# Optimization experiments

Hardware: AMD Instinct MI355X
Metric: run time of the kernel (lower is better)

Reference implementation:

```python
import jax, jax.numpy as jnp
import numpy as np

N_NODES = 30000
N_EDGES = 480000
IN_FEATS = 256
H_FEATS = 128
HEADS = 4
OUT_DIM = 128
NEG_SLOPE = 0.2  # PyG GATConv default leaky_relu slope


def gat_conv(x, src, dst, W, att_src, att_dst, bias, concat):
    """PyG-style GATConv (eval mode, self-loops already in src/dst).
    x: [N, Fin]; W: [Fin, H*C]; att_src/att_dst: [H, C]; bias: [H*C] or [C].
    """
    N = x.shape[0]
    H, C = att_src.shape
    h = (x @ W).reshape(N, H, C)                       # [N, H, C]
    a_src = jnp.einsum('nhc,hc->nh', h, att_src)       # [N, H]
    a_dst = jnp.einsum('nhc,hc->nh', h, att_dst)
    e = jax.nn.leaky_relu(a_src[src] + a_dst[dst], NEG_SLOPE)  # [E, H]
    # segment softmax over incoming edges of each dst node
    m = jax.ops.segment_max(e, dst, num_segments=N)    # [N, H]
    m = jnp.where(jnp.isfinite(m), m, 0.0)
    ex = jnp.exp(e - m[dst])
    denom = jax.ops.segment_sum(ex, dst, num_segments=N)
    alpha = ex / denom[dst]                            # [E, H]
    msg = alpha[:, :, None] * h[src]                   # [E, H, C]
    out = jax.ops.segment_sum(msg, dst, num_segments=N)  # [N, H, C]
    if concat:
        out = out.reshape(N, H * C)
    else:
        out = out.mean(axis=1)
    return out + bias


def setup_inputs() -> dict:
    key = jax.random.key(0)
    ks = jax.random.split(key, 12)
    s = 0.05
    x = jax.random.normal(ks[0], (N_NODES, IN_FEATS), dtype=jnp.float32)
    edge_index = jax.random.randint(ks[1], (2, N_EDGES), 0, N_NODES, dtype=jnp.int64)
    W1 = jax.random.normal(ks[2], (IN_FEATS, HEADS * H_FEATS), dtype=jnp.float32) * s
    att_src1 = jax.random.normal(ks[3], (HEADS, H_FEATS), dtype=jnp.float32) * s
    att_dst1 = jax.random.normal(ks[4], (HEADS, H_FEATS), dtype=jnp.float32) * s
    b1 = jnp.zeros((HEADS * H_FEATS,), dtype=jnp.float32)
    W2 = jax.random.normal(ks[5], (HEADS * H_FEATS, HEADS * H_FEATS), dtype=jnp.float32) * s
    att_src2 = jax.random.normal(ks[6], (HEADS, H_FEATS), dtype=jnp.float32) * s
    att_dst2 = jax.random.normal(ks[7], (HEADS, H_FEATS), dtype=jnp.float32) * s
    b2 = jnp.zeros((HEADS * H_FEATS,), dtype=jnp.float32)
    W3 = jax.random.normal(ks[8], (HEADS * H_FEATS, OUT_DIM), dtype=jnp.float32) * s
    att_src3 = jax.random.normal(ks[9], (1, OUT_DIM), dtype=jnp.float32) * s
    att_dst3 = jax.random.normal(ks[10], (1, OUT_DIM), dtype=jnp.float32) * s
    b3 = jnp.zeros((OUT_DIM,), dtype=jnp.float32)
    return {"x": x, "edge_index": edge_index,
            "W1": W1, "att_src1": att_src1, "att_dst1": att_dst1, "b1": b1,
            "W2": W2, "att_src2": att_src2, "att_dst2": att_dst2, "b2": b2,
            "W3": W3, "att_src3": att_src3, "att_dst3": att_dst3, "b3": b3}


def reference(x, edge_index, W1, att_src1, att_dst1, b1,
              W2, att_src2, att_dst2, b2, W3, att_src3, att_dst3, b3):
    # PyG GATConv adds self-loops by default
    loops = jnp.arange(N_NODES, dtype=edge_index.dtype)
    src = jnp.concatenate([edge_index[0], loops])
    dst = jnp.concatenate([edge_index[1], loops])
    h = gat_conv(x, src, dst, W1, att_src1, att_dst1, b1, concat=True)
    h = jax.nn.relu(h)  # dropout inactive in eval mode
    h = gat_conv(h, src, dst, W2, att_src2, att_dst2, b2, concat=True)
    h = jax.nn.relu(h)
    out = gat_conv(h, src, dst, W3, att_src3, att_dst3, b3, concat=False)
    return out
```

## Files before the change

### kernel.cpp

```cpp
#include <hip/hip_runtime.h>


#define NEG_SLOPE 0.2f

typedef __attribute__((ext_vector_type(8))) short short8;
typedef __attribute__((ext_vector_type(4))) float floatx4;

static __device__ __forceinline__ unsigned short f2bf(float f) {
    unsigned u = __float_as_uint(f);
    u = u + 0x7FFFu + ((u >> 16) & 1u);
    return (unsigned short)(u >> 16);
}
static __device__ __forceinline__ float bf2f_lo(unsigned u) {
    return __uint_as_float(u << 16);
}
static __device__ __forceinline__ float bf2f_hi(unsigned u) {
    return __uint_as_float(u & 0xFFFF0000u);
}

static __device__ __forceinline__ void async_copy16(const void* g, void* l) {
    __builtin_amdgcn_global_load_lds(
        (const __attribute__((address_space(1))) unsigned int*)g,
        (__attribute__((address_space(3))) unsigned int*)l, 16, 0, 0);
}


__global__ __launch_bounds__(256)
void cast_bf16_kernel(const float* __restrict__ in, unsigned short* __restrict__ out, int n4) {
    int i = blockIdx.x * 256 + threadIdx.x;
    if (i < n4) {
        float4 v = ((const float4*)in)[i];
        ushort4 o;
        o.x = f2bf(v.x); o.y = f2bf(v.y); o.z = f2bf(v.z); o.w = f2bf(v.w);
        ((ushort4*)out)[i] = o;
    }
}

__global__ __launch_bounds__(256)
void wt_kernel(const float* __restrict__ W, unsigned short* __restrict__ WT, int K, int N) {
    int idx = blockIdx.x * 256 + threadIdx.x;
    if (idx < K * N) {
        int k = idx / N, n = idx - k * N;
        WT[(size_t)n * K + k] = f2bf(W[idx]);
    }
}


__global__ __launch_bounds__(256)
void init_counts_kernel(int* cursor, int N) {
    int i = blockIdx.x * 256 + threadIdx.x;
    if (i < N) cursor[i] = 1;
}

__global__ __launch_bounds__(256)
void hist_kernel(const int* __restrict__ ei, int* cursor, int E) {
    int e = blockIdx.x * 256 + threadIdx.x;
    if (e < E) atomicAdd(&cursor[ei[E + e]], 1);
}

__global__ __launch_bounds__(1024)
void scan_kernel(int* __restrict__ cursor, int* __restrict__ row_ptr, int N) {
    __shared__ int wsum[16];
    __shared__ int carry_sh;
    int tid = threadIdx.x, lane = tid & 63, w = tid >> 6;
    if (tid == 0) carry_sh = 0;
    __syncthreads();
    for (int base = 0; base < N; base += 1024) {
        int i = base + tid;
        int v = (i < N) ? cursor[i] : 0;
        int x = v;
        #pragma unroll
        for (int off = 1; off < 64; off <<= 1) {
            int t = __shfl_up(x, off, 64);
            if (lane >= off) x += t;
        }
        if (lane == 63) wsum[w] = x;
        __syncthreads();
        if (w == 0 && lane < 16) {
            int y = wsum[lane];
            #pragma unroll
            for (int off = 1; off < 16; off <<= 1) {
                int t = __shfl_up(y, off, 64);
                if (lane >= off) y += t;
            }
            wsum[lane] = y;
        }
        __syncthreads();
        int woff = (w == 0) ? 0 : wsum[w - 1];
        int carry = carry_sh;
        int incl = x + woff;
        if (i < N) { int ex = carry + incl - v; row_ptr[i] = ex; cursor[i] = ex; }
        __syncthreads();
        if (tid == 1023) carry_sh = carry + incl;
        __syncthreads();
    }
    if (tid == 0) row_ptr[N] = carry_sh;
}

__global__ __launch_bounds__(256)
void scatter_kernel(const int* __restrict__ ei, int* cursor,
                    int* __restrict__ csr_src, int E, int N) {
    int i = blockIdx.x * 256 + threadIdx.x;
    if (i < E) {
        int s = ei[i], d = ei[E + i];
        int pos = atomicAdd(&cursor[d], 1);
        csr_src[pos] = s;
    } else if (i < E + N) {
        int n = i - E;
        int pos = atomicAdd(&cursor[n], 1);
        csr_src[pos] = n;
    }
}


template<bool BF16OUT>
__global__ __launch_bounds__(256)
void mfma_gemm_kernel(const unsigned short* __restrict__ A,
                      const unsigned short* __restrict__ BT,
                      void* __restrict__ C_v, int M, int Nn, int K) {
    __shared__ unsigned short As[128 * 32];
    __shared__ unsigned short Bs[128 * 32];
    const int tid = threadIdx.x;
    const int m0 = blockIdx.y * 128;
    const int n0 = blockIdx.x * 128;
    const int lane = tid & 63, wave = tid >> 6;
    const int wm = (wave & 1) * 64, wn = (wave >> 1) * 64;
    const int quad = lane >> 4, rr = lane & 15;

    const int r16 = lane >> 2;
    const int phys = lane & 3;
    const int rowL0 = wave * 32 + r16;
    const int rowL1 = wave * 32 + 16 + r16;
    const int seg0 = phys ^ ((rowL0 >> 1) & 3);
    const int seg1 = phys ^ ((rowL1 >> 1) & 3);
    const int gmA0 = min(m0 + rowL0, M - 1);
    const int gmA1 = min(m0 + rowL1, M - 1);
    const int gnB0 = n0 + rowL0;
    const int gnB1 = n0 + rowL1;
    unsigned short* ldsA0 = As + (wave * 32) * 32;
    unsigned short* ldsA1 = As + (wave * 32 + 16) * 32;
    unsigned short* ldsB0 = Bs + (wave * 32) * 32;
    unsigned short* ldsB1 = Bs + (wave * 32 + 16) * 32;

    const int swz = quad ^ ((rr >> 1) & 3);

    floatx4 acc[4][4] = {};

    for (int k0 = 0; k0 < K; k0 += 32) {
        async_copy16(A  + (size_t)gmA0 * K + k0 + seg0 * 8, ldsA0);
        async_copy16(A  + (size_t)gmA1 * K + k0 + seg1 * 8, ldsA1);
        async_copy16(BT + (size_t)gnB0 * K + k0 + seg0 * 8, ldsB0);
        async_copy16(BT + (size_t)gnB1 * K + k0 + seg1 * 8, ldsB1);
        __syncthreads();

        short8 af[4], bf[4];
        #pragma unroll
        for (int mi = 0; mi < 4; ++mi)
            af[mi] = *(const short8*)(As + (wm + mi * 16 + rr) * 32 + swz * 8);
        #pragma unroll
        for (int ni = 0; ni < 4; ++ni)
            bf[ni] = *(const short8*)(Bs + (wn + ni * 16 + rr) * 32 + swz * 8);
        #pragma unroll
        for (int mi = 0; mi < 4; ++mi)
            #pragma unroll
            for (int ni = 0; ni < 4; ++ni)
                acc[mi][ni] = __builtin_amdgcn_mfma_f32_16x16x32_bf16(
                    af[mi], bf[ni], acc[mi][ni], 0, 0, 0);
        __syncthreads();
    }

    #pragma unroll
    for (int mi = 0; mi < 4; ++mi) {
        #pragma unroll
        for (int ni = 0; ni < 4; ++ni) {
            int col = n0 + wn + ni * 16 + rr;
            #pragma unroll
            for (int r = 0; r < 4; ++r) {
                int row = m0 + wm + mi * 16 + quad * 4 + r;
                if (row < M) {
                    if (BF16OUT)
                        ((unsigned short*)C_v)[(size_t)row * Nn + col] = f2bf(acc[mi][ni][r]);
                    else
                        ((float*)C_v)[(size_t)row * Nn + col] = acc[mi][ni][r];
                }
            }
        }
    }
}


template<int H>
__global__ __launch_bounds__(256)
void attdot_kernel(const unsigned* __restrict__ hfeat, const float* __restrict__ att_src,
                   const float* __restrict__ att_dst, float* __restrict__ a_src,
                   float* __restrict__ a_dst, int N) {
    constexpr int C = 128;
    constexpr int F = H * C;
    constexpr int UPL = F / 128;
    constexpr int G = C / (2 * UPL);
    int wave = threadIdx.x >> 6, lane = threadIdx.x & 63;
    int n = blockIdx.x * 4 + wave;
    if (n >= N) return;
    const int myh = (2 * UPL * lane) / C;
    const int cbase = (2 * UPL * lane) & (C - 1);

    unsigned u[UPL];
    if (UPL == 4) {
        uint4 t = ((const uint4*)(hfeat + (size_t)n * (F / 2)))[lane];
        u[0] = t.x; u[1] = t.y; u[2] = t.z; u[3] = t.w;
    } else {
        u[0] = hfeat[(size_t)n * (F / 2) + lane];
    }
    float s = 0.f, d = 0.f;
    #pragma unroll
    for (int q = 0; q < UPL; ++q) {
        float v0 = bf2f_lo(u[q]), v1 = bf2f_hi(u[q]);
        int c = cbase + 2 * q;
        s += v0 * att_src[myh * C + c] + v1 * att_src[myh * C + c + 1];
        d += v0 * att_dst[myh * C + c] + v1 * att_dst[myh * C + c + 1];
    }
    #pragma unroll
    for (int off = G / 2; off; off >>= 1) {
        s += __shfl_xor(s, off, 64);
        d += __shfl_xor(d, off, 64);
    }
    if ((lane & (G - 1)) == 0) {
        a_src[n * H + myh] = s;
        a_dst[n * H + myh] = d;
    }
}


template<int F, int H, bool RELU, bool BF16OUT>
__global__ __launch_bounds__(256)
void agg_kernel(const unsigned* __restrict__ hfeat, const float* __restrict__ a_src,
                const float* __restrict__ a_dst, const int* __restrict__ row_ptr,
                const int* __restrict__ csr_src, const float* __restrict__ bias,
                void* __restrict__ out_v, int N) {
    constexpr int C = 128;
    constexpr int UPL = F / 128;
    constexpr int RU = F / 2;
    const int wave = threadIdx.x >> 6, lane = threadIdx.x & 63;
    const int n = blockIdx.x * 4 + wave;
    if (n >= N) return;
    const int begin = row_ptr[n];
    const int deg = row_ptr[n + 1] - begin;
    const int myh = (2 * UPL * lane) / C;
    const float adst = a_dst[n * H + myh];

    float acc[2 * UPL];
    #pragma unroll
    for (int j = 0; j < 2 * UPL; ++j) acc[j] = 0.f;
    float dacc = 0.f;

    unsigned uA[UPL], uB[UPL];
    float avA = 0.f, avB = 0.f;

#define LOADSLOT(idx, U, AV)                                              \
    {                                                                     \
        int s_ = csr_src[begin + (idx)];                                  \
        if (UPL == 4) {                                                   \
            uint4 t_ = ((const uint4*)(hfeat + (size_t)s_ * RU))[lane];   \
            U[0] = t_.x; U[1] = t_.y; U[2] = t_.z; U[3] = t_.w;           \
        } else {                                                          \
            U[0] = hfeat[(size_t)s_ * RU + lane];                         \
        }                                                                 \
        AV = a_src[s_ * H + myh];                                         \
    }

#define CONSUME(U, AV)                                                    \
    {                                                                     \
        float e_ = AV + adst;                                             \
        e_ = e_ > 0.f ? e_ : NEG_SLOPE * e_;                              \
        float ex_ = __expf(e_);                                           \
        dacc += ex_;                                                      \
        _Pragma("unroll")                                                 \
        for (int q_ = 0; q_ < UPL; ++q_) {                                \
            acc[2 * q_]     += ex_ * bf2f_lo(U[q_]);                      \
            acc[2 * q_ + 1] += ex_ * bf2f_hi(U[q_]);                      \
        }                                                                 \
    }

    LOADSLOT(0, uA, avA);
    if (deg > 1) LOADSLOT(1, uB, avB);
    int i = 0;
    for (; i + 4 <= deg; i += 2) {
        CONSUME(uA, avA);
        LOADSLOT(i + 2, uA, avA);
        CONSUME(uB, avB);
        LOADSLOT(i + 3, uB, avB);
    }
    int rem = deg - i;
    CONSUME(uA, avA);
    if (rem == 3) {
        LOADSLOT(i + 2, uA, avA);
        CONSUME(uB, avB);
        CONSUME(uA, avA);
    } else if (rem == 2) {
        CONSUME(uB, avB);
    }
#undef LOADSLOT
#undef CONSUME

    float inv = 1.f / dacc;
    const int cb = 2 * UPL * lane;
    if (BF16OUT) {
        unsigned pk[UPL];
        #pragma unroll
        for (int q = 0; q < UPL; ++q) {
            float v0 = acc[2 * q] * inv + bias[cb + 2 * q];
            float v1 = acc[2 * q + 1] * inv + bias[cb + 2 * q + 1];
            if (RELU) { v0 = fmaxf(v0, 0.f); v1 = fmaxf(v1, 0.f); }
            pk[q] = (unsigned)f2bf(v0) | ((unsigned)f2bf(v1) << 16);
        }
        if (UPL == 4) {
            uint4 t; t.x = pk[0]; t.y = pk[1]; t.z = pk[2]; t.w = pk[3];
            ((uint4*)((unsigned*)out_v + (size_t)n * RU))[lane] = t;
        } else {
            ((unsigned*)out_v)[(size_t)n * RU + lane] = pk[0];
        }
    } else {
        #pragma unroll
        for (int q = 0; q < UPL; ++q) {
            float v0 = acc[2 * q] * inv + bias[cb + 2 * q];
            float v1 = acc[2 * q + 1] * inv + bias[cb + 2 * q + 1];
            if (RELU) { v0 = fmaxf(v0, 0.f); v1 = fmaxf(v1, 0.f); }
            float2 o; o.x = v0; o.y = v1;
            ((float2*)((float*)out_v + (size_t)n * F))[UPL * lane + q] = o;
        }
    }
}


extern "C" void kernel_launch(void* const* d_in, const int* in_sizes, int n_in,
                              void* d_out, int out_size, void* d_ws, size_t ws_size,
                              hipStream_t stream) {
    const float* x        = (const float*)d_in[0];
    const int*   ei       = (const int*)  d_in[1];
    const float* W1       = (const float*)d_in[2];
    const float* att_src1 = (const float*)d_in[3];
    const float* att_dst1 = (const float*)d_in[4];
    const float* b1       = (const float*)d_in[5];
    const float* W2       = (const float*)d_in[6];
    const float* att_src2 = (const float*)d_in[7];
    const float* att_dst2 = (const float*)d_in[8];
    const float* b2       = (const float*)d_in[9];
    const float* W3       = (const float*)d_in[10];
    const float* att_src3 = (const float*)d_in[11];
    const float* att_dst3 = (const float*)d_in[12];
    const float* b3       = (const float*)d_in[13];

    const int IN_FEATS = 256;
    const int N = in_sizes[0] / IN_FEATS;
    const int E = in_sizes[1] / 2;
    const int ET = E + N;

    char* p = (char*)d_ws;
    unsigned short* h_bf    = (unsigned short*)p; p += (size_t)N * 512 * sizeof(unsigned short);
    unsigned short* act_bf  = (unsigned short*)p; p += (size_t)N * 512 * sizeof(unsigned short);
    unsigned short* x_bf    = (unsigned short*)p; p += (size_t)N * 256 * sizeof(unsigned short);
    float*          a_src   = (float*)p;          p += (size_t)N * 4 * sizeof(float);
    float*          a_dst   = (float*)p;          p += (size_t)N * 4 * sizeof(float);
    unsigned short* W_T     = (unsigned short*)p; p += (size_t)512 * 512 * sizeof(unsigned short);
    int*            row_ptr = (int*)p;            p += ((size_t)N + 16) * sizeof(int);
    int*            cursor  = (int*)p;            p += ((size_t)N + 16) * sizeof(int);
    int*            csr_src = (int*)p;            p += (size_t)ET * sizeof(int);

    init_counts_kernel<<<(N + 255) / 256, 256, 0, stream>>>(cursor, N);
    hist_kernel<<<(E + 255) / 256, 256, 0, stream>>>(ei, cursor, E);
    scan_kernel<<<1, 1024, 0, stream>>>(cursor, row_ptr, N);
    scatter_kernel<<<(E + N + 255) / 256, 256, 0, stream>>>(ei, cursor, csr_src, E, N);

    {
        int n4 = N * 256 / 4;
        cast_bf16_kernel<<<(n4 + 255) / 256, 256, 0, stream>>>(x, x_bf, n4);
    }

    const int MB = (N + 127) / 128;
    const int NB4 = (N + 3) / 4;

    wt_kernel<<<(256 * 512 + 255) / 256, 256, 0, stream>>>(W1, W_T, 256, 512);
    mfma_gemm_kernel<true><<<dim3(4, MB), 256, 0, stream>>>(x_bf, W_T, h_bf, N, 512, 256);
    attdot_kernel<4><<<NB4, 256, 0, stream>>>((const unsigned*)h_bf, att_src1, att_dst1, a_src, a_dst, N);
    agg_kernel<512, 4, true, true><<<NB4, 256, 0, stream>>>((const unsigned*)h_bf, a_src, a_dst, row_ptr, csr_src, b1, act_bf, N);

    wt_kernel<<<(512 * 512 + 255) / 256, 256, 0, stream>>>(W2, W_T, 512, 512);
    mfma_gemm_kernel<true><<<dim3(4, MB), 256, 0, stream>>>(act_bf, W_T, h_bf, N, 512, 512);
    attdot_kernel<4><<<NB4, 256, 0, stream>>>((const unsigned*)h_bf, att_src2, att_dst2, a_src, a_dst, N);
    agg_kernel<512, 4, true, true><<<NB4, 256, 0, stream>>>((const unsigned*)h_bf, a_src, a_dst, row_ptr, csr_src, b2, act_bf, N);

    wt_kernel<<<(512 * 128 + 255) / 256, 256, 0, stream>>>(W3, W_T, 512, 128);
    mfma_gemm_kernel<true><<<dim3(1, MB), 256, 0, stream>>>(act_bf, W_T, h_bf, N, 128, 512);
    attdot_kernel<1><<<NB4, 256, 0, stream>>>((const unsigned*)h_bf, att_src3, att_dst3, a_src, a_dst, N);
    agg_kernel<128, 1, false, false><<<NB4, 256, 0, stream>>>((const unsigned*)h_bf, a_src, a_dst, row_ptr, csr_src, b3, d_out, N);
}
```

Measured before the change: 448.8 us.

## Parallelize CSR scan, fuse attention dots into GEMM, deepen aggregation prefetch

Replaces the single-block serial prefix scan with a three-kernel multi-block scan (block sums, block offsets, final scan). Fuses the attention-coefficient dot products into the GEMM epilogue using fp32 accumulators, which removes the attdot kernels and their re-read of h. In the aggregation kernel, neighbour prefetch grows from two slots to four, and scalar readfirstlane is applied to row pointers and source indices. The block-offset kernel assumes at most 64 scan blocks, and the fused epilogue adds shared memory and shuffle work to the GEMM.

```diff
diff --git a/kernel.cpp b/kernel.cpp
--- a/kernel.cpp
+++ b/kernel.cpp
@@ -59,42 +59,66 @@
 }
 
 __global__ __launch_bounds__(1024)
-void scan_kernel(int* __restrict__ cursor, int* __restrict__ row_ptr, int N) {
+void scan_bsum_kernel(const int* __restrict__ cursor, int* __restrict__ bsum, int N) {
     __shared__ int wsum[16];
-    __shared__ int carry_sh;
     int tid = threadIdx.x, lane = tid & 63, w = tid >> 6;
-    if (tid == 0) carry_sh = 0;
+    int i = blockIdx.x * 1024 + tid;
+    int v = (i < N) ? cursor[i] : 0;
+    #pragma unroll
+    for (int off = 32; off; off >>= 1) v += __shfl_xor(v, off, 64);
+    if (lane == 0) wsum[w] = v;
     __syncthreads();
-    for (int base = 0; base < N; base += 1024) {
-        int i = base + tid;
-        int v = (i < N) ? cursor[i] : 0;
-        int x = v;
-        #pragma unroll
-        for (int off = 1; off < 64; off <<= 1) {
-            int t = __shfl_up(x, off, 64);
-            if (lane >= off) x += t;
-        }
-        if (lane == 63) wsum[w] = x;
-        __syncthreads();
-        if (w == 0 && lane < 16) {
-            int y = wsum[lane];
-            #pragma unroll
-            for (int off = 1; off < 16; off <<= 1) {
-                int t = __shfl_up(y, off, 64);
-                if (lane >= off) y += t;
-            }
-            wsum[lane] = y;
-        }
-        __syncthreads();
-        int woff = (w == 0) ? 0 : wsum[w - 1];
-        int carry = carry_sh;
-        int incl = x + woff;
-        if (i < N) { int ex = carry + incl - v; row_ptr[i] = ex; cursor[i] = ex; }
-        __syncthreads();
-        if (tid == 1023) carry_sh = carry + incl;
-        __syncthreads();
-    }
-    if (tid == 0) row_ptr[N] = carry_sh;
+    if (tid == 0) {
+        int t = 0;
+        #pragma unroll
+        for (int k = 0; k < 16; ++k) t += wsum[k];
+        bsum[blockIdx.x] = t;
+    }
+}
+
+__global__ __launch_bounds__(64)
+void scan_boffs_kernel(const int* __restrict__ bsum, int* __restrict__ boffs,
+                       int NB, int* __restrict__ row_ptr, int N) {
+    int lane = threadIdx.x;
+    int v = (lane < NB) ? bsum[lane] : 0;
+    int x = v;
+    #pragma unroll
+    for (int off = 1; off < 64; off <<= 1) {
+        int t = __shfl_up(x, off, 64);
+        if (lane >= off) x += t;
+    }
+    if (lane < NB) boffs[lane] = x - v;
+    if (lane == 63) row_ptr[N] = x;
+}
+
+__global__ __launch_bounds__(1024)
+void scan_final_kernel(int* __restrict__ cursor, const int* __restrict__ boffs,
+                       int* __restrict__ row_ptr, int N) {
+    __shared__ int wsum[16];
+    int tid = threadIdx.x, lane = tid & 63, w = tid >> 6;
+    int i = blockIdx.x * 1024 + tid;
+    int v = (i < N) ? cursor[i] : 0;
+    int x = v;
+    #pragma unroll
+    for (int off = 1; off < 64; off <<= 1) {
+        int t = __shfl_up(x, off, 64);
+        if (lane >= off) x += t;
+    }
+    if (lane == 63) wsum[w] = x;
+    __syncthreads();
+    if (w == 0 && lane < 16) {
+        int y = wsum[lane];
+        #pragma unroll
+        for (int off = 1; off < 16; off <<= 1) {
+            int t = __shfl_up(y, off, 64);
+            if (lane >= off) y += t;
+        }
+        wsum[lane] = y;
+    }
+    __syncthreads();
+    int woff = (w == 0) ? 0 : wsum[w - 1];
+    int ex = boffs[blockIdx.x] + woff + x - v;
+    if (i < N) { row_ptr[i] = ex; cursor[i] = ex; }
 }
 
 __global__ __launch_bounds__(256)
@@ -113,16 +137,22 @@
 }
 
 
-template<bool BF16OUT>
 __global__ __launch_bounds__(256)
 void mfma_gemm_kernel(const unsigned short* __restrict__ A,
                       const unsigned short* __restrict__ BT,
-                      void* __restrict__ C_v, int M, int Nn, int K) {
+                      unsigned short* __restrict__ C,
+                      const float* __restrict__ att_src,
+                      const float* __restrict__ att_dst,
+                      float* __restrict__ a_srcO, float* __restrict__ a_dstO,
+                      int H, int M, int Nn, int K) {
     __shared__ unsigned short As[128 * 32];
     __shared__ unsigned short Bs[128 * 32];
+    __shared__ float psum[2][128];
+    __shared__ float pdsum[2][128];
     const int tid = threadIdx.x;
     const int m0 = blockIdx.y * 128;
     const int n0 = blockIdx.x * 128;
+    const int head = blockIdx.x;
     const int lane = tid & 63, wave = tid >> 6;
     const int wm = (wave & 1) * 64, wn = (wave >> 1) * 64;
     const int quad = lane >> 4, rr = lane & 15;
@@ -177,56 +207,48 @@
             #pragma unroll
             for (int r = 0; r < 4; ++r) {
                 int row = m0 + wm + mi * 16 + quad * 4 + r;
-                if (row < M) {
-                    if (BF16OUT)
-                        ((unsigned short*)C_v)[(size_t)row * Nn + col] = f2bf(acc[mi][ni][r]);
-                    else
-                        ((float*)C_v)[(size_t)row * Nn + col] = acc[mi][ni][r];
-                }
+                if (row < M) C[(size_t)row * Nn + col] = f2bf(acc[mi][ni][r]);
             }
         }
     }
-}
-
-
-template<int H>
-__global__ __launch_bounds__(256)
-void attdot_kernel(const unsigned* __restrict__ hfeat, const float* __restrict__ att_src,
-                   const float* __restrict__ att_dst, float* __restrict__ a_src,
-                   float* __restrict__ a_dst, int N) {
-    constexpr int C = 128;
-    constexpr int F = H * C;
-    constexpr int UPL = F / 128;
-    constexpr int G = C / (2 * UPL);
-    int wave = threadIdx.x >> 6, lane = threadIdx.x & 63;
-    int n = blockIdx.x * 4 + wave;
-    if (n >= N) return;
-    const int myh = (2 * UPL * lane) / C;
-    const int cbase = (2 * UPL * lane) & (C - 1);
-
-    unsigned u[UPL];
-    if (UPL == 4) {
-        uint4 t = ((const uint4*)(hfeat + (size_t)n * (F / 2)))[lane];
-        u[0] = t.x; u[1] = t.y; u[2] = t.z; u[3] = t.w;
-    } else {
-        u[0] = hfeat[(size_t)n * (F / 2) + lane];
-    }
-    float s = 0.f, d = 0.f;
-    #pragma unroll
-    for (int q = 0; q < UPL; ++q) {
-        float v0 = bf2f_lo(u[q]), v1 = bf2f_hi(u[q]);
-        int c = cbase + 2 * q;
-        s += v0 * att_src[myh * C + c] + v1 * att_src[myh * C + c + 1];
-        d += v0 * att_dst[myh * C + c] + v1 * att_dst[myh * C + c + 1];
-    }
-    #pragma unroll
-    for (int off = G / 2; off; off >>= 1) {
-        s += __shfl_xor(s, off, 64);
-        d += __shfl_xor(d, off, 64);
-    }
-    if ((lane & (G - 1)) == 0) {
-        a_src[n * H + myh] = s;
-        a_dst[n * H + myh] = d;
+
+    float ats[4], atd[4];
+    #pragma unroll
+    for (int ni = 0; ni < 4; ++ni) {
+        int c = wn + ni * 16 + rr;
+        ats[ni] = att_src[head * 128 + c];
+        atd[ni] = att_dst[head * 128 + c];
+    }
+    const int wnh = wn >> 6;
+    #pragma unroll
+    for (int mi = 0; mi < 4; ++mi) {
+        #pragma unroll
+        for (int r = 0; r < 4; ++r) {
+            float ps = 0.f, pd = 0.f;
+            #pragma unroll
+            for (int ni = 0; ni < 4; ++ni) {
+                ps += ats[ni] * acc[mi][ni][r];
+                pd += atd[ni] * acc[mi][ni][r];
+            }
+            #pragma unroll
+            for (int off = 1; off < 16; off <<= 1) {
+                ps += __shfl_xor(ps, off, 64);
+                pd += __shfl_xor(pd, off, 64);
+            }
+            if (rr == 0) {
+                int row = wm + mi * 16 + quad * 4 + r;
+                psum[wnh][row] = ps;
+                pdsum[wnh][row] = pd;
+            }
+        }
+    }
+    __syncthreads();
+    if (tid < 128) {
+        int gr = m0 + tid;
+        if (gr < M) {
+            a_srcO[(size_t)gr * H + head] = psum[0][tid] + psum[1][tid];
+            a_dstO[(size_t)gr * H + head] = pdsum[0][tid] + pdsum[1][tid];
+        }
     }
 }
 
@@ -243,8 +265,8 @@
     const int wave = threadIdx.x >> 6, lane = threadIdx.x & 63;
     const int n = blockIdx.x * 4 + wave;
     if (n >= N) return;
-    const int begin = row_ptr[n];
-    const int deg = row_ptr[n + 1] - begin;
+    const int begin = __builtin_amdgcn_readfirstlane(row_ptr[n]);
+    const int deg = __builtin_amdgcn_readfirstlane(row_ptr[n + 1]) - begin;
     const int myh = (2 * UPL * lane) / C;
     const float adst = a_dst[n * H + myh];
 
@@ -253,12 +275,12 @@
     for (int j = 0; j < 2 * UPL; ++j) acc[j] = 0.f;
     float dacc = 0.f;
 
-    unsigned uA[UPL], uB[UPL];
-    float avA = 0.f, avB = 0.f;
+    unsigned u0[UPL], u1[UPL], u2[UPL], u3[UPL];
+    float av0 = 0.f, av1 = 0.f, av2 = 0.f, av3 = 0.f;
 
 #define LOADSLOT(idx, U, AV)                                              \
     {                                                                     \
-        int s_ = csr_src[begin + (idx)];                                  \
+        int s_ = __builtin_amdgcn_readfirstlane(csr_src[begin + (idx)]);  \
         if (UPL == 4) {                                                   \
             uint4 t_ = ((const uint4*)(hfeat + (size_t)s_ * RU))[lane];   \
             U[0] = t_.x; U[1] = t_.y; U[2] = t_.z; U[3] = t_.w;           \
@@ -281,24 +303,25 @@
         }                                                                 \
     }
 
-    LOADSLOT(0, uA, avA);
-    if (deg > 1) LOADSLOT(1, uB, avB);
+    LOADSLOT(0, u0, av0);
+    if (deg > 1) LOADSLOT(1, u1, av1);
+    if (deg > 2) LOADSLOT(2, u2, av2);
+    if (deg > 3) LOADSLOT(3, u3, av3);
     int i = 0;
-    for (; i + 4 <= deg; i += 2) {
-        CONSUME(uA, avA);
-        LOADSLOT(i + 2, uA, avA);
-        CONSUME(uB, avB);
-        LOADSLOT(i + 3, uB, avB);
+    for (; i + 8 <= deg; i += 4) {
+        CONSUME(u0, av0); LOADSLOT(i + 4, u0, av0);
+        CONSUME(u1, av1); LOADSLOT(i + 5, u1, av1);
+        CONSUME(u2, av2); LOADSLOT(i + 6, u2, av2);
+        CONSUME(u3, av3); LOADSLOT(i + 7, u3, av3);
     }
     int rem = deg - i;
-    CONSUME(uA, avA);
-    if (rem == 3) {
-        LOADSLOT(i + 2, uA, avA);
-        CONSUME(uB, avB);
-        CONSUME(uA, avA);
-    } else if (rem == 2) {
-        CONSUME(uB, avB);
-    }
+    CONSUME(u0, av0); if (rem > 4) LOADSLOT(i + 4, u0, av0);
+    if (rem > 1) { CONSUME(u1, av1); if (rem > 5) LOADSLOT(i + 5, u1, av1); }
+    if (rem > 2) { CONSUME(u2, av2); if (rem > 6) LOADSLOT(i + 6, u2, av2); }
+    if (rem > 3) CONSUME(u3, av3);
+    if (rem > 4) CONSUME(u0, av0);
+    if (rem > 5) CONSUME(u1, av1);
+    if (rem > 6) CONSUME(u2, av2);
 #undef LOADSLOT
 #undef CONSUME
 
@@ -354,6 +377,7 @@
     const int N = in_sizes[0] / IN_FEATS;
     const int E = in_sizes[1] / 2;
     const int ET = E + N;
+    const int NB = (N + 1023) / 1024;
 
     char* p = (char*)d_ws;
     unsigned short* h_bf    = (unsigned short*)p; p += (size_t)N * 512 * sizeof(unsigned short);
@@ -364,11 +388,15 @@
     unsigned short* W_T     = (unsigned short*)p; p += (size_t)512 * 512 * sizeof(unsigned short);
     int*            row_ptr = (int*)p;            p += ((size_t)N + 16) * sizeof(int);
     int*            cursor  = (int*)p;            p += ((size_t)N + 16) * sizeof(int);
+    int*            bsum    = (int*)p;            p += 64 * sizeof(int);
+    int*            boffs   = (int*)p;            p += 64 * sizeof(int);
     int*            csr_src = (int*)p;            p += (size_t)ET * sizeof(int);
 
     init_counts_kernel<<<(N + 255) / 256, 256, 0, stream>>>(cursor, N);
     hist_kernel<<<(E + 255) / 256, 256, 0, stream>>>(ei, cursor, E);
-    scan_kernel<<<1, 1024, 0, stream>>>(cursor, row_ptr, N);
+    scan_bsum_kernel<<<NB, 1024, 0, stream>>>(cursor, bsum, N);
+    scan_boffs_kernel<<<1, 64, 0, stream>>>(bsum, boffs, NB, row_ptr, N);
+    scan_final_kernel<<<NB, 1024, 0, stream>>>(cursor, boffs, row_ptr, N);
     scatter_kernel<<<(E + N + 255) / 256, 256, 0, stream>>>(ei, cursor, csr_src, E, N);
 
     {
@@ -380,17 +408,14 @@
     const int NB4 = (N + 3) / 4;
 
     wt_kernel<<<(256 * 512 + 255) / 256, 256, 0, stream>>>(W1, W_T, 256, 512);
-    mfma_gemm_kernel<true><<<dim3(4, MB), 256, 0, stream>>>(x_bf, W_T, h_bf, N, 512, 256);
-    attdot_kernel<4><<<NB4, 256, 0, stream>>>((const unsigned*)h_bf, att_src1, att_dst1, a_src, a_dst, N);
+    mfma_gemm_kernel<<<dim3(4, MB), 256, 0, stream>>>(x_bf, W_T, h_bf, att_src1, att_dst1, a_src, a_dst, 4, N, 512, 256);
     agg_kernel<512, 4, true, true><<<NB4, 256, 0, stream>>>((const unsigned*)h_bf, a_src, a_dst, row_ptr, csr_src, b1, act_bf, N);
 
     wt_kernel<<<(512 * 512 + 255) / 256, 256, 0, stream>>>(W2, W_T, 512, 512);
-    mfma_gemm_kernel<true><<<dim3(4, MB), 256, 0, stream>>>(act_bf, W_T, h_bf, N, 512, 512);
-    attdot_kernel<4><<<NB4, 256, 0, stream>>>((const unsigned*)h_bf, att_src2, att_dst2, a_src, a_dst, N);
+    mfma_gemm_kernel<<<dim3(4, MB), 256, 0, stream>>>(act_bf, W_T, h_bf, att_src2, att_dst2, a_src, a_dst, 4, N, 512, 512);
     agg_kernel<512, 4, true, true><<<NB4, 256, 0, stream>>>((const unsigned*)h_bf, a_src, a_dst, row_ptr, csr_src, b2, act_bf, N);
 
     wt_kernel<<<(512 * 128 + 255) / 256, 256, 0, stream>>>(W3, W_T, 512, 128);
-    mfma_gemm_kernel<true><<<dim3(1, MB), 256, 0, stream>>>(act_bf, W_T, h_bf, N, 128, 512);
-    attdot_kernel<1><<<NB4, 256, 0, stream>>>((const unsigned*)h_bf, att_src3, att_dst3, a_src, a_dst, N);
+    mfma_gemm_kernel<<<dim3(1, MB), 256, 0, stream>>>(act_bf, W_T, h_bf, att_src3, att_dst3, a_src, a_dst, 1, N, 128, 512);
     agg_kernel<128, 1, false, false><<<NB4, 256, 0, stream>>>((const unsigned*)h_bf, a_src, a_dst, row_ptr, csr_src, b3, d_out, N);
 }
```

After: 422.5 us. 5.8% less time.
